# Kernel optimization log

Hardware: AMD Instinct MI355X
Metric: run time of the kernel (lower is better)

The kernel has to match this reference:

```python
import jax, jax.numpy as jnp
import numpy as np

COST_BBOX = 1.0
COST_GIOU = 1.0
TOPK = 5


def _make_boxes(key, b, n):
    # valid xyxy boxes in [0,1]: centers + small positive sizes
    kc, ks = jax.random.split(key)
    cxy = jax.random.uniform(kc, (b, n, 2))
    wh = jax.random.uniform(ks, (b, n, 2)) * 0.2 + 0.01
    return jnp.concatenate([cxy - wh / 2, cxy + wh / 2], axis=-1)


def setup_inputs() -> dict:
    key = jax.random.key(0)
    k1, k2, k3, k4 = jax.random.split(key, 4)
    B, NP, NG = 8, 5000, 300
    return {
        "pred_box": _make_boxes(k1, B, NP),
        "pred_obj": jax.random.normal(k3, (B, NP), dtype=jnp.float32),
        "gt_box": _make_boxes(k2, B, NG),
        "gt_obj": jax.random.normal(k4, (B, NG), dtype=jnp.float32),
    }


def pairwise_giou(pb, gb):
    # pb: [B,N,4], gb: [B,M,4] in xyxy -> giou [B,N,M]
    area_p = (pb[..., 2] - pb[..., 0]) * (pb[..., 3] - pb[..., 1])  # [B,N]
    area_g = (gb[..., 2] - gb[..., 0]) * (gb[..., 3] - gb[..., 1])  # [B,M]
    lt = jnp.maximum(pb[:, :, None, :2], gb[:, None, :, :2])  # [B,N,M,2]
    rb = jnp.minimum(pb[:, :, None, 2:], gb[:, None, :, 2:])
    wh = jnp.clip(rb - lt, 0.0)
    inter = wh[..., 0] * wh[..., 1]                                  # [B,N,M]
    union = area_p[:, :, None] + area_g[:, None, :] - inter
    iou = inter / union
    # smallest enclosing box
    lt_e = jnp.minimum(pb[:, :, None, :2], gb[:, None, :, :2])
    rb_e = jnp.maximum(pb[:, :, None, 2:], gb[:, None, :, 2:])
    wh_e = jnp.clip(rb_e - lt_e, 0.0)
    area_e = wh_e[..., 0] * wh_e[..., 1]
    return iou - (area_e - union) / area_e


def cost_matrix(pred_box, gt_box):
    # L1 cdist: [B,N,M]
    cost_bbox = jnp.sum(jnp.abs(pred_box[:, :, None, :] - gt_box[:, None, :, :]), axis=-1)
    cost_giou = 1.0 - pairwise_giou(pred_box, gt_box)
    return COST_BBOX * cost_bbox + COST_GIOU * cost_giou


def reference(pred_box, pred_obj, gt_box, gt_obj):
    C = cost_matrix(pred_box, gt_box)            # [B, N_pred, N_gt]
    Ct = jnp.swapaxes(C, 1, 2)                   # [B, N_gt, N_pred]
    _, idx = jax.lax.top_k(-Ct, TOPK)            # smallest-cost preds per gt: [B, N_gt, TOPK]
    B, M, _ = idx.shape
    matched_pred = idx.reshape(B, M * TOPK).astype(jnp.int32)
    matched_gt = jnp.broadcast_to(jnp.repeat(jnp.arange(M, dtype=jnp.int32), TOPK)[None, :], (B, M * TOPK))
    return matched_pred, matched_gt
```

## Files before the change

### kernel.cpp

```cpp
#include <hip/hip_runtime.h>

#pragma clang fp contract(off)

typedef unsigned long long u64;

#define TOPK 5
#define WAVES 4

#define CE(x, y) do { if ((y) < (x)) { u64 _t = (x); (x) = (y); (y) = _t; } } while (0)

#define INSERT(nk, k0, k1, k2, k3, k4)                          \
    do { if ((nk) < k4) {                                       \
        if ((nk) < k3) { k4 = k3;                               \
            if ((nk) < k2) { k3 = k2;                           \
                if ((nk) < k1) { k2 = k1;                       \
                    if ((nk) < k0) { k1 = k0; k0 = (nk); }      \
                    else           { k1 = (nk); }               \
                } else { k2 = (nk); }                           \
            } else { k3 = (nk); }                               \
        } else { k4 = (nk); }                                   \
    } } while (0)

__device__ __forceinline__ float fast_div(float a, float b) {
    float r = __builtin_amdgcn_rcpf(b);
    r = fmaf(fmaf(-b, r, 1.0f), r, r);
    float q = a * r;
    q = fmaf(fmaf(-b, q, a), r, q);
    return q;
}

__device__ __forceinline__ u64 eval_key(const float4 pb, const float area_p,
                                        const float4 gb, const float g_area,
                                        const int p) {
    const float cost_bbox = fabsf(pb.x - gb.x) + fabsf(pb.y - gb.y)
                          + fabsf(pb.z - gb.z) + fabsf(pb.w - gb.w);
    const float ltx = fmaxf(pb.x, gb.x), lty = fmaxf(pb.y, gb.y);
    const float rbx = fminf(pb.z, gb.z), rby = fminf(pb.w, gb.w);
    const float iw = fmaxf(rbx - ltx, 0.0f), ih = fmaxf(rby - lty, 0.0f);
    const float inter = iw * ih;
    const float uni = area_p + g_area - inter;
    const float iou = fast_div(inter, uni);
    const float ex1 = fminf(pb.x, gb.x), ey1 = fminf(pb.y, gb.y);
    const float ex2 = fmaxf(pb.z, gb.z), ey2 = fmaxf(pb.w, gb.w);
    const float area_e = (ex2 - ex1) * (ey2 - ey1);
    const float giou = iou - fast_div(area_e - uni, area_e);
    const float cost = cost_bbox + (1.0f - giou);
    return ((u64)__float_as_uint(cost) << 32) | (unsigned)p;
}

__global__ __launch_bounds__(64 * WAVES) void matcher_topk_kernel(
    const float* __restrict__ pred_box,
    const float* __restrict__ gt_box,
    int* __restrict__ out_pred,
    int* __restrict__ out_gt,
    int B, int NP, int NG)
{
    const int pairsPerB = (NG + 1) >> 1;
    const int tp = blockIdx.x;
    const int b  = tp / pairsPerB;
    const int j  = tp - b * pairsPerB;
    const int m0 = 2 * j;
    const int m1 = m0 + 1;
    const bool has1 = (m1 < NG);

    const int wid  = threadIdx.x >> 6;
    const int lane = threadIdx.x & 63;

    const float4 gb0 = ((const float4*)gt_box)[b * NG + m0];
    const float4 gb1 = ((const float4*)gt_box)[b * NG + (has1 ? m1 : m0)];
    const float ga0 = (gb0.z - gb0.x) * (gb0.w - gb0.y);
    const float ga1 = (gb1.z - gb1.x) * (gb1.w - gb1.y);

    u64 a0 = ~0ULL, a1 = ~0ULL, a2 = ~0ULL, a3 = ~0ULL, a4 = ~0ULL;
    u64 c0 = ~0ULL, c1 = ~0ULL, c2 = ~0ULL, c3 = ~0ULL, c4 = ~0ULL;

    const float4* pbase = (const float4*)pred_box + (size_t)b * NP;

    int p = threadIdx.x;
    for (; p + 256 < NP; p += 512) {
        const float4 pA = pbase[p];
        const float4 pB = pbase[p + 256];
        const float apA = (pA.z - pA.x) * (pA.w - pA.y);
        const float apB = (pB.z - pB.x) * (pB.w - pB.y);
        const u64 kA0 = eval_key(pA, apA, gb0, ga0, p);
        const u64 kB0 = eval_key(pB, apB, gb0, ga0, p + 256);
        const u64 kA1 = eval_key(pA, apA, gb1, ga1, p);
        const u64 kB1 = eval_key(pB, apB, gb1, ga1, p + 256);
        INSERT(kA0, a0, a1, a2, a3, a4);
        INSERT(kB0, a0, a1, a2, a3, a4);
        INSERT(kA1, c0, c1, c2, c3, c4);
        INSERT(kB1, c0, c1, c2, c3, c4);
    }
    if (p < NP) {
        const float4 pA = pbase[p];
        const float apA = (pA.z - pA.x) * (pA.w - pA.y);
        const u64 kA0 = eval_key(pA, apA, gb0, ga0, p);
        const u64 kA1 = eval_key(pA, apA, gb1, ga1, p);
        INSERT(kA0, a0, a1, a2, a3, a4);
        INSERT(kA1, c0, c1, c2, c3, c4);
    }

    #pragma unroll
    for (int off = 1; off < 64; off <<= 1) {
        const u64 sa0 = __shfl_xor(a0, off);
        const u64 sa1 = __shfl_xor(a1, off);
        const u64 sa2 = __shfl_xor(a2, off);
        const u64 sa3 = __shfl_xor(a3, off);
        const u64 sa4 = __shfl_xor(a4, off);
        const u64 sc0 = __shfl_xor(c0, off);
        const u64 sc1 = __shfl_xor(c1, off);
        const u64 sc2 = __shfl_xor(c2, off);
        const u64 sc3 = __shfl_xor(c3, off);
        const u64 sc4 = __shfl_xor(c4, off);

        u64 x0 = a0 < sa4 ? a0 : sa4;
        u64 x1 = a1 < sa3 ? a1 : sa3;
        u64 x2 = a2 < sa2 ? a2 : sa2;
        u64 x3 = a3 < sa1 ? a3 : sa1;
        u64 x4 = a4 < sa0 ? a4 : sa0;
        CE(x0, x1); CE(x3, x4); CE(x2, x4); CE(x2, x3); CE(x1, x4);
        CE(x0, x3); CE(x0, x2); CE(x1, x3); CE(x1, x2);
        a0 = x0; a1 = x1; a2 = x2; a3 = x3; a4 = x4;

        u64 y0 = c0 < sc4 ? c0 : sc4;
        u64 y1 = c1 < sc3 ? c1 : sc3;
        u64 y2 = c2 < sc2 ? c2 : sc2;
        u64 y3 = c3 < sc1 ? c3 : sc1;
        u64 y4 = c4 < sc0 ? c4 : sc0;
        CE(y0, y1); CE(y3, y4); CE(y2, y4); CE(y2, y3); CE(y1, y4);
        CE(y0, y3); CE(y0, y2); CE(y1, y3); CE(y1, y2);
        c0 = y0; c1 = y1; c2 = y2; c3 = y3; c4 = y4;
    }

    __shared__ u64 lds[2][WAVES][TOPK];
    if (lane == 0) {
        lds[0][wid][0] = a0; lds[0][wid][1] = a1; lds[0][wid][2] = a2;
        lds[0][wid][3] = a3; lds[0][wid][4] = a4;
        lds[1][wid][0] = c0; lds[1][wid][1] = c1; lds[1][wid][2] = c2;
        lds[1][wid][3] = c3; lds[1][wid][4] = c4;
    }
    __syncthreads();

    if (threadIdx.x < 2) {
        const int which = threadIdx.x;
        if (which == 0 || has1) {
            const int m = m0 + which;
            int head[WAVES];
            #pragma unroll
            for (int w = 0; w < WAVES; ++w) head[w] = 0;
            const int base = (b * NG + m) * TOPK;
            #pragma unroll
            for (int r = 0; r < TOPK; ++r) {
                u64 best = ~0ULL; int bw = 0;
                #pragma unroll
                for (int w = 0; w < WAVES; ++w) {
                    const u64 v = lds[which][w][head[w]];
                    if (v < best) { best = v; bw = w; }
                }
                head[bw]++;
                out_pred[base + r] = (int)(unsigned)(best & 0xFFFFFFFFu);
                out_gt[base + r]   = m;
            }
        }
    }
}

extern "C" void kernel_launch(void* const* d_in, const int* in_sizes, int n_in,
                              void* d_out, int out_size, void* d_ws, size_t ws_size,
                              hipStream_t stream) {
    const float* pred_box = (const float*)d_in[0];
    const float* gt_box   = (const float*)d_in[2];

    const int NP = 5000;
    const int B  = in_sizes[1] / NP;
    const int NG = in_sizes[3] / B;

    int* out_pred = (int*)d_out;
    int* out_gt   = out_pred + B * NG * TOPK;

    const int pairsPerB = (NG + 1) >> 1;
    const int blocks = B * pairsPerB;
    hipLaunchKernelGGL(matcher_topk_kernel, dim3(blocks), dim3(64 * WAVES), 0, stream,
                       pred_box, gt_box, out_pred, out_gt, B, NP, NG);
}
```

Before: 40.44 us.

## Double-buffer pred loads with inline asm and use branchless sort-merge top-k

Each wave now scans its own contiguous quarter of the predictions in groups of 256. Loads are issued with inline-asm global_load_dwordx4 into two register sets, and explicit vmcnt waits overlap the next group's memory traffic with the current group's GIoU math. The branchy per-key insertion is replaced by a branchless 4-key sorting network merged into the running top-5. This removes divergence and load stalls but adds many 64-bit compare/select ops per key, where the old insertion usually exited after one compare. It also relies on NP being divisible by 4 and on manual waitcnt correctness.

```diff
diff --git a/kernel.cpp b/kernel.cpp
--- a/kernel.cpp
+++ b/kernel.cpp
@@ -3,23 +3,13 @@
 #pragma clang fp contract(off)
 
 typedef unsigned long long u64;
+typedef float f4 __attribute__((ext_vector_type(4)));
 
 #define TOPK 5
 #define WAVES 4
 
-#define CE(x, y) do { if ((y) < (x)) { u64 _t = (x); (x) = (y); (y) = _t; } } while (0)
-
-#define INSERT(nk, k0, k1, k2, k3, k4)                          \
-    do { if ((nk) < k4) {                                       \
-        if ((nk) < k3) { k4 = k3;                               \
-            if ((nk) < k2) { k3 = k2;                           \
-                if ((nk) < k1) { k2 = k1;                       \
-                    if ((nk) < k0) { k1 = k0; k0 = (nk); }      \
-                    else           { k1 = (nk); }               \
-                } else { k2 = (nk); }                           \
-            } else { k3 = (nk); }                               \
-        } else { k4 = (nk); }                                   \
-    } } while (0)
+#define CE(x, y) do { const u64 _a = (x), _b = (y); const bool _l = _b < _a; \
+                      (x) = _l ? _b : _a; (y) = _l ? _a : _b; } while (0)
 
 __device__ __forceinline__ float fast_div(float a, float b) {
     float r = __builtin_amdgcn_rcpf(b);
@@ -29,8 +19,8 @@
     return q;
 }
 
-__device__ __forceinline__ u64 eval_key(const float4 pb, const float area_p,
-                                        const float4 gb, const float g_area,
+__device__ __forceinline__ u64 eval_one(const f4 pb, const float area_p,
+                                        const f4 gb, const float g_area,
                                         const int p) {
     const float cost_bbox = fabsf(pb.x - gb.x) + fabsf(pb.y - gb.y)
                           + fabsf(pb.z - gb.z) + fabsf(pb.w - gb.w);
@@ -60,45 +50,109 @@
     const int b  = tp / pairsPerB;
     const int j  = tp - b * pairsPerB;
     const int m0 = 2 * j;
-    const int m1 = m0 + 1;
-    const bool has1 = (m1 < NG);
+    const bool has1 = (m0 + 1 < NG);
 
     const int wid  = threadIdx.x >> 6;
     const int lane = threadIdx.x & 63;
 
-    const float4 gb0 = ((const float4*)gt_box)[b * NG + m0];
-    const float4 gb1 = ((const float4*)gt_box)[b * NG + (has1 ? m1 : m0)];
+    const f4 gb0 = ((const f4*)gt_box)[b * NG + m0];
+    const f4 gb1 = ((const f4*)gt_box)[b * NG + (has1 ? m0 + 1 : m0)];
     const float ga0 = (gb0.z - gb0.x) * (gb0.w - gb0.y);
     const float ga1 = (gb1.z - gb1.x) * (gb1.w - gb1.y);
 
+    const int NPm1  = NP - 1;
+    const int quart = NP >> 2;
+    const int wbase = wid * quart;
+    const int ngroups = (quart + 255) >> 8;
+
     u64 a0 = ~0ULL, a1 = ~0ULL, a2 = ~0ULL, a3 = ~0ULL, a4 = ~0ULL;
     u64 c0 = ~0ULL, c1 = ~0ULL, c2 = ~0ULL, c3 = ~0ULL, c4 = ~0ULL;
 
-    const float4* pbase = (const float4*)pred_box + (size_t)b * NP;
-
-    int p = threadIdx.x;
-    for (; p + 256 < NP; p += 512) {
-        const float4 pA = pbase[p];
-        const float4 pB = pbase[p + 256];
-        const float apA = (pA.z - pA.x) * (pA.w - pA.y);
-        const float apB = (pB.z - pB.x) * (pB.w - pB.y);
-        const u64 kA0 = eval_key(pA, apA, gb0, ga0, p);
-        const u64 kB0 = eval_key(pB, apB, gb0, ga0, p + 256);
-        const u64 kA1 = eval_key(pA, apA, gb1, ga1, p);
-        const u64 kB1 = eval_key(pB, apB, gb1, ga1, p + 256);
-        INSERT(kA0, a0, a1, a2, a3, a4);
-        INSERT(kB0, a0, a1, a2, a3, a4);
-        INSERT(kA1, c0, c1, c2, c3, c4);
-        INSERT(kB1, c0, c1, c2, c3, c4);
-    }
-    if (p < NP) {
-        const float4 pA = pbase[p];
-        const float apA = (pA.z - pA.x) * (pA.w - pA.y);
-        const u64 kA0 = eval_key(pA, apA, gb0, ga0, p);
-        const u64 kA1 = eval_key(pA, apA, gb1, ga1, p);
-        INSERT(kA0, a0, a1, a2, a3, a4);
-        INSERT(kA1, c0, c1, c2, c3, c4);
-    }
+    const f4* pbase = (const f4*)pred_box + (size_t)b * NP;
+
+#define GLOAD(g, rA, rB, rC, rD) do {                                        \
+    const int _i = wbase + ((g) << 8) + lane;                                \
+    const f4* _p0 = pbase + min(_i,       NPm1);                             \
+    const f4* _p1 = pbase + min(_i + 64,  NPm1);                             \
+    const f4* _p2 = pbase + min(_i + 128, NPm1);                             \
+    const f4* _p3 = pbase + min(_i + 192, NPm1);                             \
+    asm volatile("global_load_dwordx4 %0, %1, off" : "=v"(rA) : "v"(_p0));   \
+    asm volatile("global_load_dwordx4 %0, %1, off" : "=v"(rB) : "v"(_p1));   \
+    asm volatile("global_load_dwordx4 %0, %1, off" : "=v"(rC) : "v"(_p2));   \
+    asm volatile("global_load_dwordx4 %0, %1, off" : "=v"(rD) : "v"(_p3));   \
+} while (0)
+
+#define GWAIT() do {                                   \
+    asm volatile("s_waitcnt vmcnt(4)");                \
+    __builtin_amdgcn_sched_barrier(0);                 \
+} while (0)
+
+#define SORT4_MERGE(kA, kB, kC, kD, s0, s1, s2, s3, s4) do {                 \
+    CE(kA, kB); CE(kC, kD); CE(kA, kC); CE(kB, kD); CE(kB, kC);              \
+    u64 n0 = s0;                                                             \
+    u64 n1 = s1 < kD ? s1 : kD;                                              \
+    u64 n2 = s2 < kC ? s2 : kC;                                              \
+    u64 n3 = s3 < kB ? s3 : kB;                                              \
+    u64 n4 = s4 < kA ? s4 : kA;                                              \
+    CE(n0, n1); CE(n3, n4); CE(n2, n4); CE(n2, n3); CE(n1, n4);              \
+    CE(n0, n3); CE(n0, n2); CE(n1, n3); CE(n1, n2);                          \
+    s0 = n0; s1 = n1; s2 = n2; s3 = n3; s4 = n4;                             \
+} while (0)
+
+#define PROCG(g, rA, rB, rC, rD) do {                                        \
+    const int _li = ((g) << 8) + lane;                                       \
+    const int _gi = wbase + _li;                                             \
+    const float apA = (rA.z - rA.x) * (rA.w - rA.y);                         \
+    const float apB = (rB.z - rB.x) * (rB.w - rB.y);                         \
+    const float apC = (rC.z - rC.x) * (rC.w - rC.y);                         \
+    const float apD = (rD.z - rD.x) * (rD.w - rD.y);                         \
+    u64 kA0 = eval_one(rA, apA, gb0, ga0, _gi);                              \
+    u64 kB0 = eval_one(rB, apB, gb0, ga0, _gi + 64);                         \
+    u64 kC0 = eval_one(rC, apC, gb0, ga0, _gi + 128);                        \
+    u64 kD0 = eval_one(rD, apD, gb0, ga0, _gi + 192);                        \
+    u64 kA1 = eval_one(rA, apA, gb1, ga1, _gi);                              \
+    u64 kB1 = eval_one(rB, apB, gb1, ga1, _gi + 64);                         \
+    u64 kC1 = eval_one(rC, apC, gb1, ga1, _gi + 128);                        \
+    u64 kD1 = eval_one(rD, apD, gb1, ga1, _gi + 192);                        \
+    if ((g) == ngroups - 1) {           \
+        kA0 = (_li       < quart) ? kA0 : ~0ULL;                             \
+        kB0 = (_li + 64  < quart) ? kB0 : ~0ULL;                             \
+        kC0 = (_li + 128 < quart) ? kC0 : ~0ULL;                             \
+        kD0 = (_li + 192 < quart) ? kD0 : ~0ULL;                             \
+        kA1 = (_li       < quart) ? kA1 : ~0ULL;                             \
+        kB1 = (_li + 64  < quart) ? kB1 : ~0ULL;                             \
+        kC1 = (_li + 128 < quart) ? kC1 : ~0ULL;                             \
+        kD1 = (_li + 192 < quart) ? kD1 : ~0ULL;                             \
+    }                                                                        \
+    SORT4_MERGE(kA0, kB0, kC0, kD0, a0, a1, a2, a3, a4);                     \
+    SORT4_MERGE(kA1, kB1, kC1, kD1, c0, c1, c2, c3, c4);                     \
+} while (0)
+
+    f4 eA, eB, eC, eD;
+    f4 oA, oB, oC, oD;
+
+    GLOAD(0, eA, eB, eC, eD);
+    GLOAD(1, oA, oB, oC, oD);
+
+    for (int g = 0; g < ngroups; g += 2) {
+        GWAIT();
+        PROCG(g, eA, eB, eC, eD);
+        GLOAD(g + 2, eA, eB, eC, eD);
+        if (g + 1 < ngroups) {
+            GWAIT();
+            PROCG(g + 1, oA, oB, oC, oD);
+            GLOAD(g + 3, oA, oB, oC, oD);
+        }
+    }
+
+    asm volatile("s_waitcnt vmcnt(0)");
+    __builtin_amdgcn_sched_barrier(0);
+    asm volatile("" :: "v"(eA), "v"(eB), "v"(eC), "v"(eD),
+                       "v"(oA), "v"(oB), "v"(oC), "v"(oD));
+
+#undef GLOAD
+#undef GWAIT
+#undef PROCG
 
     #pragma unroll
     for (int off = 1; off < 64; off <<= 1) {
@@ -118,48 +172,47 @@
         u64 x2 = a2 < sa2 ? a2 : sa2;
         u64 x3 = a3 < sa1 ? a3 : sa1;
         u64 x4 = a4 < sa0 ? a4 : sa0;
-        CE(x0, x1); CE(x3, x4); CE(x2, x4); CE(x2, x3); CE(x1, x4);
-        CE(x0, x3); CE(x0, x2); CE(x1, x3); CE(x1, x2);
-        a0 = x0; a1 = x1; a2 = x2; a3 = x3; a4 = x4;
-
         u64 y0 = c0 < sc4 ? c0 : sc4;
         u64 y1 = c1 < sc3 ? c1 : sc3;
         u64 y2 = c2 < sc2 ? c2 : sc2;
         u64 y3 = c3 < sc1 ? c3 : sc1;
         u64 y4 = c4 < sc0 ? c4 : sc0;
+        CE(x0, x1); CE(x3, x4); CE(x2, x4); CE(x2, x3); CE(x1, x4);
+        CE(x0, x3); CE(x0, x2); CE(x1, x3); CE(x1, x2);
         CE(y0, y1); CE(y3, y4); CE(y2, y4); CE(y2, y3); CE(y1, y4);
         CE(y0, y3); CE(y0, y2); CE(y1, y3); CE(y1, y2);
+        a0 = x0; a1 = x1; a2 = x2; a3 = x3; a4 = x4;
         c0 = y0; c1 = y1; c2 = y2; c3 = y3; c4 = y4;
     }
 
-    __shared__ u64 lds[2][WAVES][TOPK];
+    __shared__ u64 smerge[WAVES][2][TOPK];
     if (lane == 0) {
-        lds[0][wid][0] = a0; lds[0][wid][1] = a1; lds[0][wid][2] = a2;
-        lds[0][wid][3] = a3; lds[0][wid][4] = a4;
-        lds[1][wid][0] = c0; lds[1][wid][1] = c1; lds[1][wid][2] = c2;
-        lds[1][wid][3] = c3; lds[1][wid][4] = c4;
+        smerge[wid][0][0] = a0; smerge[wid][0][1] = a1; smerge[wid][0][2] = a2;
+        smerge[wid][0][3] = a3; smerge[wid][0][4] = a4;
+        smerge[wid][1][0] = c0; smerge[wid][1][1] = c1; smerge[wid][1][2] = c2;
+        smerge[wid][1][3] = c3; smerge[wid][1][4] = c4;
     }
     __syncthreads();
 
     if (threadIdx.x < 2) {
         const int which = threadIdx.x;
         if (which == 0 || has1) {
-            const int m = m0 + which;
+            const int mm = m0 + which;
             int head[WAVES];
             #pragma unroll
             for (int w = 0; w < WAVES; ++w) head[w] = 0;
-            const int base = (b * NG + m) * TOPK;
+            const int baseo = (b * NG + mm) * TOPK;
             #pragma unroll
             for (int r = 0; r < TOPK; ++r) {
                 u64 best = ~0ULL; int bw = 0;
                 #pragma unroll
                 for (int w = 0; w < WAVES; ++w) {
-                    const u64 v = lds[which][w][head[w]];
+                    const u64 v = smerge[w][which][head[w]];
                     if (v < best) { best = v; bw = w; }
                 }
                 head[bw]++;
-                out_pred[base + r] = (int)(unsigned)(best & 0xFFFFFFFFu);
-                out_gt[base + r]   = m;
+                out_pred[baseo + r] = (int)(unsigned)(best & 0xFFFFFFFFu);
+                out_gt[baseo + r]   = mm;
             }
         }
     }
```

Measured after the change: 42.88 us. 6.0% more time.
